# Kernel optimization log

Hardware: AMD Instinct MI355X
Metric: run time of the kernel (lower is better)

Reference implementation:

```python
import jax, jax.numpy as jnp
import numpy as np

L = 7          # num_gc_layers
H = 64         # hidden_channels
N = 100000     # nodes
E = 1000000    # edges
G = 512        # graphs in batch
ATOM_DIMS = [119, 5, 12, 12, 10, 6, 6, 2, 2]   # OGB full_atom_feature_dims
BOND_DIMS = [5, 6, 2]                          # OGB full_bond_feature_dims
EPS_GEN = 1e-7   # GENConv message eps
EPS_BN = 1e-5    # BatchNorm eps
ATOM_OFF = np.concatenate([[0], np.cumsum(ATOM_DIMS)[:-1]]).astype(np.int64)
BOND_OFF = np.concatenate([[0], np.cumsum(BOND_DIMS)[:-1]]).astype(np.int64)


def setup_inputs() -> dict:
    key = jax.random.key(0)
    ks = jax.random.split(key, 12)
    x = jax.random.randint(ks[0], (N, len(ATOM_DIMS)), 0, 2)
    edge_index = jax.random.randint(ks[1], (2, E), 0, N)
    edge_attr = jax.random.randint(ks[2], (E, len(BOND_DIMS)), 0, 2)
    batch = jnp.sort(jax.random.randint(ks[3], (N,), 0, G))
    s = 0.02
    w = 1.0 / np.sqrt(H).astype(np.float32)
    return {
        "atom_table": jax.random.normal(ks[4], (sum(ATOM_DIMS), H), jnp.float32) * s,
        "bond_table": jax.random.normal(ks[5], (sum(BOND_DIMS), H), jnp.float32) * s,
        "vn0": jnp.zeros((H,), jnp.float32),  # virtualnode embedding, const-init 0
        "gcn_W": jax.random.normal(ks[6], (L, H, H), jnp.float32) * w,
        "gcn_b": jnp.zeros((L, H), jnp.float32),
        "norm_gamma": jnp.ones((L, H), jnp.float32),
        "norm_beta": jnp.zeros((L, H), jnp.float32),
        "vn_W1": jax.random.normal(ks[7], (L - 1, H, H), jnp.float32) * w,
        "vn_b1": jnp.zeros((L - 1, H), jnp.float32),
        "vn_g1": jnp.ones((L - 1, H), jnp.float32),
        "vn_be1": jnp.zeros((L - 1, H), jnp.float32),
        "vn_W2": jax.random.normal(ks[8], (L - 1, H, H), jnp.float32) * w,
        "vn_b2": jnp.zeros((L - 1, H), jnp.float32),
        "vn_g2": jnp.ones((L - 1, H), jnp.float32),
        "vn_be2": jnp.zeros((L - 1, H), jnp.float32),
        "x": x,
        "edge_index": edge_index,
        "edge_attr": edge_attr,
        "batch": batch,
        "classification": 0,
    }


def _bn(h, g, b):
    # BatchNorm1d, training mode (biased batch stats over the node axis)
    mu = h.mean(0)
    var = h.var(0)
    return (h - mu) * jax.lax.rsqrt(var + EPS_BN) * g + b


def _genconv(h, src, dst, edge_emb, W, b):
    # GENConv, aggr='add', mlp_layers=1 (single last_lin Linear)
    msg = jax.nn.relu(h[src] + edge_emb) + EPS_GEN        # [E, H]
    m = jax.ops.segment_sum(msg, dst, num_segments=N)     # [N, H]
    return (h + m) @ W + b


def reference(atom_table, bond_table, vn0, gcn_W, gcn_b, norm_gamma, norm_beta,
              vn_W1, vn_b1, vn_g1, vn_be1, vn_W2, vn_b2, vn_g2, vn_be2,
              x, edge_index, edge_attr, batch, classification):
    # AtomEncoder / BondEncoder: sum of per-feature embeddings via offset table
    h = atom_table[x + jnp.asarray(ATOM_OFF)].sum(1)                   # [N, H]
    edge_emb = bond_table[edge_attr + jnp.asarray(BOND_OFF)].sum(1)    # [E, H]
    vn = jnp.broadcast_to(vn0[None, :], (G, H))                        # [G, H]
    h = h + vn[batch]
    src, dst = edge_index[0], edge_index[1]

    # block == 'res+': conv0, then [BN -> ReLU -> (vnode) -> conv -> +res]
    h = _genconv(h, src, dst, edge_emb, gcn_W[0], gcn_b[0])
    for l in range(1, L):
        h2 = jax.nn.relu(_bn(h, norm_gamma[l - 1], norm_beta[l - 1]))
        # virtual-node update: global_add_pool + 2-layer MLP (Lin-BN-ReLU x2)
        vt = jax.ops.segment_sum(h2, batch, num_segments=G) + vn
        z = jax.nn.relu(_bn(vt @ vn_W1[l - 1] + vn_b1[l - 1], vn_g1[l - 1], vn_be1[l - 1]))
        vn = jax.nn.relu(_bn(z @ vn_W2[l - 1] + vn_b2[l - 1], vn_g2[l - 1], vn_be2[l - 1]))
        h2 = h2 + vn[batch]
        h = _genconv(h2, src, dst, edge_emb, gcn_W[l], gcn_b[l]) + h
    h = _bn(h, norm_gamma[L - 1], norm_beta[L - 1])

    # classification=False -> global_mean_pool readout
    cnt = jax.ops.segment_sum(jnp.ones((N,), h.dtype), batch, num_segments=G)
    out = jax.ops.segment_sum(h, batch, num_segments=G) / jnp.clip(cnt, 1.0)[:, None]
    return out
```

## Files before the change

### kernel.cpp

```cpp
#include <hip/hip_runtime.h>
#include <hip/hip_bf16.h>
#include <hip/hip_fp16.h>

#define NN 100000
#define EE 1000000
#define GG 512
#define HH 64
#define LL 7
#define NH (NN*HH)
#define GH (GG*HH)
#define EPS_GEN 1e-7f
#define EPS_BN 1e-5f
#define SCAN_BLKS 98
#define SLOTS 64
#define CONV_BLOCKS 6250

typedef _Float16 half8  __attribute__((ext_vector_type(8)));
typedef _Float16 half4  __attribute__((ext_vector_type(4)));
typedef _Float16 half2v __attribute__((ext_vector_type(2)));
typedef float    float4v __attribute__((ext_vector_type(4)));

__device__ __constant__ int c_atom_off[9] = {0,119,124,136,148,158,164,170,172};

__global__ void k_atom_enc(const float* __restrict__ atom_table,
                           const float* __restrict__ vn0,
                           const int* __restrict__ x,
                           _Float16* __restrict__ h16) {
    int tid = blockIdx.x * blockDim.x + threadIdx.x;
    int n = tid >> 6, c = tid & 63;
    if (n >= NN) return;
    float acc = vn0[c];
    const int* xr = x + n * 9;
    #pragma unroll
    for (int f = 0; f < 9; ++f) acc += atom_table[(xr[f] + c_atom_off[f]) * HH + c];
    h16[tid] = (_Float16)acc;
}

__global__ void k_prep(const float* __restrict__ W, const float* __restrict__ bond,
                       _Float16* __restrict__ W16f, _Float16* __restrict__ ctab16) {
    int i = blockIdx.x * blockDim.x + threadIdx.x;
    if (i < LL * 4096) {
        int l = i / 4096, r = i % 4096;
        int j = r & 7, lane = (r >> 3) & 63, kh = (r >> 9) & 1, t = r >> 10;
        int q = (lane >> 4) & 3, c = lane & 15;
        W16f[i] = (_Float16)W[l * 4096 + (kh * 32 + q * 8 + j) * 64 + t * 16 + c];
    } else {
        int k = i - LL * 4096;
        if (k < 60 * 64) {
            int cmb = k >> 6, lane = k & 63;
            int a0 = cmb % 5, a1 = (cmb / 5) % 6, a2 = cmb / 30;
            ctab16[k] = (_Float16)(bond[a0 * 64 + lane] + bond[(5 + a1) * 64 + lane]
                                   + bond[(11 + a2) * 64 + lane]);
        }
    }
}

__global__ void k_count2(const int* __restrict__ edge_index, const int* __restrict__ edge_attr,
                         int* __restrict__ cur, unsigned int* __restrict__ recs) {
    int e = blockIdx.x * blockDim.x + threadIdx.x;
    if (e >= EE) return;
    int src = edge_index[e];
    int dst = edge_index[EE + e];
    int combo = edge_attr[e * 3] + 5 * edge_attr[e * 3 + 1] + 30 * edge_attr[e * 3 + 2];
    unsigned int rank = (unsigned int)atomicAdd(&cur[dst], 1);
    recs[e] = (unsigned int)src | ((unsigned int)combo << 17) | (rank << 23);
}

__global__ void k_scan1(const int* __restrict__ cnt, int* __restrict__ rp, int* __restrict__ part) {
    __shared__ int s[256];
    int t = threadIdx.x, blk = blockIdx.x;
    int base = blk * 1024 + t * 4;
    int v0 = 0, v1 = 0, v2 = 0, v3 = 0;
    if (base + 3 < NN) {
        int4 q = *(const int4*)(cnt + base);
        v0 = q.x; v1 = q.y; v2 = q.z; v3 = q.w;
    } else {
        if (base + 0 < NN) v0 = cnt[base + 0];
        if (base + 1 < NN) v1 = cnt[base + 1];
        if (base + 2 < NN) v2 = cnt[base + 2];
        if (base + 3 < NN) v3 = cnt[base + 3];
    }
    int s4 = v0 + v1 + v2 + v3;
    s[t] = s4;
    __syncthreads();
    for (int off = 1; off < 256; off <<= 1) {
        int x = (t >= off) ? s[t - off] : 0;
        __syncthreads();
        s[t] += x;
        __syncthreads();
    }
    int excl = s[t] - s4;
    if (t == 255) part[blk] = s[255];
    if (base + 0 < NN) rp[base + 0] = excl;
    if (base + 1 < NN) rp[base + 1] = excl + v0;
    if (base + 2 < NN) rp[base + 2] = excl + v0 + v1;
    if (base + 3 < NN) rp[base + 3] = excl + v0 + v1 + v2;
}

__global__ void k_scan2(int* __restrict__ part) {
    __shared__ int s[128];
    int t = threadIdx.x;
    int v = (t < SCAN_BLKS) ? part[t] : 0;
    s[t] = v;
    __syncthreads();
    for (int off = 1; off < 128; off <<= 1) {
        int x = (t >= off) ? s[t - off] : 0;
        __syncthreads();
        s[t] += x;
        __syncthreads();
    }
    if (t < SCAN_BLKS) part[t] = s[t] - v;
}

__global__ void k_scan3(int* __restrict__ rp, const int* __restrict__ part) {
    int i = blockIdx.x * blockDim.x + threadIdx.x;
    if (i < NN) rp[i] += part[i >> 10];
    if (i == 0) rp[NN] = EE;
}

__global__ void k_fill2(const int* __restrict__ edge_index, const unsigned int* __restrict__ recs,
                        const int* __restrict__ rp, unsigned int* __restrict__ edges) {
    int e = blockIdx.x * blockDim.x + threadIdx.x;
    if (e >= EE) return;
    unsigned int rec = recs[e];
    int dst = edge_index[EE + e];
    edges[rp[dst] + (rec >> 23)] = rec & 0x7FFFFFu;
}

__global__ __launch_bounds__(128, 8) void k_conv_mfma(
        const _Float16* __restrict__ h16, const float* res,
        const int* __restrict__ rp, const unsigned int* __restrict__ edges,
        const _Float16* __restrict__ ctab16, const _Float16* __restrict__ W16f,
        const float* __restrict__ bvec,
        float* __restrict__ out, float* __restrict__ statsPart) {
    __shared__ __align__(16) _Float16 sA[16 * 64];
    int lane = threadIdx.x & 63;
    int wv = threadIdx.x >> 6;
    int g  = lane >> 5;
    int sg = (lane >> 4) & 1;
    int cc = (lane & 15) * 4;
    int q = lane >> 4;
    int c = lane & 15;
    int n0 = blockIdx.x * 16;
    const half4 z4 = {(_Float16)0, (_Float16)0, (_Float16)0, (_Float16)0};

    const half8* wf = (const half8*)W16f;
    half8 bf[2][2];
    #pragma unroll
    for (int t = 0; t < 2; ++t) {
        bf[t][0] = wf[((wv * 2 + t) * 2 + 0) * 64 + lane];
        bf[t][1] = wf[((wv * 2 + t) * 2 + 1) * 64 + lane];
    }

    #pragma unroll 1
    for (int i = 0; i < 4; ++i) {
        int r_loc = wv * 8 + g * 4 + i;
        int n = n0 + r_loc;
        float ax = 0.f, ay = 0.f, az = 0.f, aw = 0.f;
        int beg = rp[n], end = rp[n + 1];
        int deg = end - beg;
        int j = beg;
        for (; j + 8 <= end; j += 8) {
            unsigned int rec[4];
            rec[0] = edges[j + sg];
            rec[1] = edges[j + 2 + sg];
            rec[2] = edges[j + 4 + sg];
            rec[3] = edges[j + 6 + sg];
            half4 hh[4], tt[4];
            #pragma unroll
            for (int u = 0; u < 4; ++u) {
                hh[u] = *(const half4*)(h16 + (size_t)(rec[u] & 0x1FFFF) * 64 + cc);
                tt[u] = *(const half4*)(ctab16 + ((rec[u] >> 17) & 63) * 64 + cc);
            }
            #pragma unroll
            for (int u = 0; u < 4; ++u) {
                half4 m = __builtin_elementwise_max(hh[u] + tt[u], z4);
                ax += (float)m[0]; ay += (float)m[1];
                az += (float)m[2]; aw += (float)m[3];
            }
        }
        for (; j < end; j += 4) {
            int i0 = j + sg, i1 = j + 2 + sg;
            bool v0 = i0 < end, v1 = i1 < end;
            unsigned int r0 = edges[v0 ? i0 : beg];
            unsigned int r1 = edges[v1 ? i1 : beg];
            half4 h0 = *(const half4*)(h16 + (size_t)(r0 & 0x1FFFF) * 64 + cc);
            half4 t0 = *(const half4*)(ctab16 + ((r0 >> 17) & 63) * 64 + cc);
            half4 h1 = *(const half4*)(h16 + (size_t)(r1 & 0x1FFFF) * 64 + cc);
            half4 t1 = *(const half4*)(ctab16 + ((r1 >> 17) & 63) * 64 + cc);
            half4 m0 = __builtin_elementwise_max(h0 + t0, z4);
            half4 m1 = __builtin_elementwise_max(h1 + t1, z4);
            if (v0) {
                ax += (float)m0[0]; ay += (float)m0[1];
                az += (float)m0[2]; aw += (float)m0[3];
            }
            if (v1) {
                ax += (float)m1[0]; ay += (float)m1[1];
                az += (float)m1[2]; aw += (float)m1[3];
            }
        }
        ax += __shfl_xor(ax, 16, 64); ay += __shfl_xor(ay, 16, 64);
        az += __shfl_xor(az, 16, 64); aw += __shfl_xor(aw, 16, 64);
        half4 sv = *(const half4*)(h16 + (size_t)n * 64 + cc);
        float ed = (float)deg * EPS_GEN;
        ax += (float)sv[0] + ed; ay += (float)sv[1] + ed;
        az += (float)sv[2] + ed; aw += (float)sv[3] + ed;
        if (sg == 0) {
            half4 pk;
            pk[0] = (_Float16)ax; pk[1] = (_Float16)ay;
            pk[2] = (_Float16)az; pk[3] = (_Float16)aw;
            *(half4*)(&sA[r_loc * 64 + cc]) = pk;
        }
    }
    __syncthreads();

    half8 af0 = *(const half8*)(sA + c * 64 + q * 8);
    half8 af1 = *(const half8*)(sA + c * 64 + 32 + q * 8);
    float4v d[2];
    #pragma unroll
    for (int t = 0; t < 2; ++t) {
        d[t] = (float4v){0.f, 0.f, 0.f, 0.f};
        d[t] = __builtin_amdgcn_mfma_f32_16x16x32_f16(af0, bf[t][0], d[t], 0, 0, 0);
        d[t] = __builtin_amdgcn_mfma_f32_16x16x32_f16(af1, bf[t][1], d[t], 0, 0, 0);
    }

    float ps[2], pq[2];
    #pragma unroll
    for (int t = 0; t < 2; ++t) { ps[t] = 0.f; pq[t] = 0.f; }
    #pragma unroll
    for (int t = 0; t < 2; ++t) {
        int tg = wv * 2 + t;
        float bz = bvec[tg * 16 + c];
        #pragma unroll
        for (int r = 0; r < 4; ++r) {
            int row = n0 + q * 4 + r;
            float val = d[t][r] + bz;
            size_t off = (size_t)row * 64 + tg * 16 + c;
            if (res) val += res[off];
            out[off] = val;
            ps[t] += val;
            pq[t] = fmaf(val, val, pq[t]);
        }
    }
    #pragma unroll
    for (int t = 0; t < 2; ++t) {
        ps[t] += __shfl_xor(ps[t], 16, 64); ps[t] += __shfl_xor(ps[t], 32, 64);
        pq[t] += __shfl_xor(pq[t], 16, 64); pq[t] += __shfl_xor(pq[t], 32, 64);
    }
    float* sp = statsPart + ((blockIdx.x * 2 + wv) & (SLOTS - 1)) * 128;
    if (lane < 16) {
        #pragma unroll
        for (int t = 0; t < 2; ++t) {
            int tg = wv * 2 + t;
            atomicAdd(&sp[tg * 16 + lane], ps[t]);
            atomicAdd(&sp[64 + tg * 16 + lane], pq[t]);
        }
    }
}


__global__ void k_bn_relu_vt2(const float* __restrict__ h, const float* __restrict__ spart,
                              const float* __restrict__ gamma, const float* __restrict__ beta,
                              const int* __restrict__ batch,
                              _Float16* __restrict__ h16, float* __restrict__ vt) {
    __shared__ float sTmp[256];
    __shared__ float sMS[128];
    {
        int ch = threadIdx.x & 127, hf = threadIdx.x >> 7;
        float a = 0.f;
        #pragma unroll 8
        for (int i = hf; i < SLOTS; i += 2) a += spart[i * 128 + ch];
        sTmp[threadIdx.x] = a;
    }
    __syncthreads();
    if (threadIdx.x < 64) {
        int c = threadIdx.x;
        float s = sTmp[c] + sTmp[128 + c];
        float q = sTmp[64 + c] + sTmp[192 + c];
        float mu = s * (1.f / NN);
        float var = q * (1.f / NN) - mu * mu;
        sMS[c] = mu;
        sMS[64 + c] = rsqrtf(var + EPS_BN);
    }
    __syncthreads();
    int lane = threadIdx.x & 63;
    int w = blockIdx.x * 4 + (threadIdx.x >> 6);
    int n0 = w * 8;
    if (n0 >= NN) return;
    int n1 = min(n0 + 8, NN);
    float mu = sMS[lane];
    float inv = sMS[64 + lane] * gamma[lane];
    float bet = beta[lane];
    float acc = 0.f;
    int gcur = batch[n0];
    for (int n = n0; n < n1; ++n) {
        float v = fmaxf((h[(size_t)n * 64 + lane] - mu) * inv + bet, 0.f);
        h16[(size_t)n * 64 + lane] = (_Float16)v;
        int g = batch[n];
        if (g != gcur) {
            atomicAdd(&vt[(size_t)gcur * 64 + lane], acc);
            acc = 0.f; gcur = g;
        }
        acc += v;
    }
    atomicAdd(&vt[(size_t)gcur * 64 + lane], acc);
}

__global__ void k_vn_gemm(float* __restrict__ in, int clear_in,
                          const float* in_stats, const float* in_g, const float* in_be,
                          const float* addmat, const float* add_stats,
                          const float* add_g, const float* add_be,
                          const float* addvec,
                          const float* __restrict__ W, const float* __restrict__ bvec,
                          float* __restrict__ out, float* __restrict__ out_stats) {
    __shared__ float sW[4096];
    __shared__ float sRed[2][4][64];
    for (int i = threadIdx.x; i < 4096; i += 256) sW[i] = W[i];
    __syncthreads();
    int lane = threadIdx.x & 63, wv = threadIdx.x >> 6;
    int w = blockIdx.x * 4 + wv;
    float imu = 0.f, iinv = 0.f, ibe = 0.f;
    if (in_stats) {
        float mu = in_stats[lane] * (1.f / GG);
        float var = in_stats[64 + lane] * (1.f / GG) - mu * mu;
        imu = mu; iinv = rsqrtf(var + EPS_BN) * in_g[lane]; ibe = in_be[lane];
    }
    float amu = 0.f, ainv = 0.f, abe = 0.f;
    if (addmat && add_stats) {
        float mu = add_stats[lane] * (1.f / GG);
        float var = add_stats[64 + lane] * (1.f / GG) - mu * mu;
        amu = mu; ainv = rsqrtf(var + EPS_BN) * add_g[lane]; abe = add_be[lane];
    }
    float av_const = addvec ? addvec[lane] : 0.f;
    float psum = 0.f, psq = 0.f;
    for (int r = w * 4; r < w * 4 + 4; ++r) {
        float va = in[r * 64 + lane];
        if (clear_in) in[r * 64 + lane] = 0.f;
        if (in_stats) va = fmaxf((va - imu) * iinv + ibe, 0.f);
        if (addmat) va += fmaxf((addmat[r * 64 + lane] - amu) * ainv + abe, 0.f);
        va += av_const;
        float acc = bvec[lane];
        #pragma unroll
        for (int k = 0; k < 64; ++k)
            acc = fmaf(__shfl(va, k, 64), sW[k * 64 + lane], acc);
        out[r * 64 + lane] = acc;
        psum += acc; psq = fmaf(acc, acc, psq);
    }
    sRed[0][wv][lane] = psum;
    sRed[1][wv][lane] = psq;
    __syncthreads();
    if (threadIdx.x < 64) {
        float s = 0.f, q = 0.f;
        #pragma unroll
        for (int i = 0; i < 4; ++i) { s += sRed[0][i][threadIdx.x]; q += sRed[1][i][threadIdx.x]; }
        atomicAdd(&out_stats[threadIdx.x], s);
        atomicAdd(&out_stats[64 + threadIdx.x], q);
    }
}

__global__ void k_addvn16(_Float16* __restrict__ h16, const float* __restrict__ t2,
                          const float* __restrict__ stats,
                          const float* __restrict__ g2, const float* __restrict__ be2,
                          const int* __restrict__ batch) {
    int tid = blockIdx.x * blockDim.x + threadIdx.x;
    int n = tid >> 4, p = tid & 15;
    if (n >= NN) return;
    int c0 = p * 4;
    float mu[4], iv[4], be[4];
    #pragma unroll
    for (int k = 0; k < 4; ++k) {
        int ci = c0 + k;
        float m = stats[ci] * (1.f / GG);
        float v = stats[64 + ci] * (1.f / GG) - m * m;
        mu[k] = m;
        iv[k] = rsqrtf(v + EPS_BN) * g2[ci];
        be[k] = be2[ci];
    }
    int g = batch[n];
    float4 t = *(const float4*)(t2 + (size_t)g * 64 + c0);
    float tv[4] = {t.x, t.y, t.z, t.w};
    half4 hv = *(half4*)(h16 + (size_t)n * 64 + c0);
    half4 o;
    #pragma unroll
    for (int k = 0; k < 4; ++k) {
        float a = fmaxf((tv[k] - mu[k]) * iv[k] + be[k], 0.f);
        o[k] = (_Float16)((float)hv[k] + a);
    }
    *(half4*)(h16 + (size_t)n * 64 + c0) = o;
}

__global__ void k_pool2(const float* __restrict__ h, const float* __restrict__ spart,
                        const float* __restrict__ gamma, const float* __restrict__ beta,
                        const int* __restrict__ batch,
                        float* __restrict__ out, float* __restrict__ cnt) {
    __shared__ float sTmp[256];
    __shared__ float sMS[128];
    {
        int ch = threadIdx.x & 127, hf = threadIdx.x >> 7;
        float a = 0.f;
        #pragma unroll 8
        for (int i = hf; i < SLOTS; i += 2) a += spart[i * 128 + ch];
        sTmp[threadIdx.x] = a;
    }
    __syncthreads();
    if (threadIdx.x < 64) {
        int c = threadIdx.x;
        float s = sTmp[c] + sTmp[128 + c];
        float q = sTmp[64 + c] + sTmp[192 + c];
        float mu = s * (1.f / NN);
        float var = q * (1.f / NN) - mu * mu;
        sMS[c] = mu;
        sMS[64 + c] = rsqrtf(var + EPS_BN);
    }
    __syncthreads();
    int lane = threadIdx.x & 63;
    int w = blockIdx.x * 4 + (threadIdx.x >> 6);
    int n0 = w * 16;
    if (n0 >= NN) return;
    int n1 = min(n0 + 16, NN);
    float mu = sMS[lane];
    float inv = sMS[64 + lane] * gamma[lane];
    float bet = beta[lane];
    float acc = 0.f;
    int run = 0;
    int gcur = batch[n0];
    for (int n = n0; n < n1; ++n) {
        float v = (h[(size_t)n * 64 + lane] - mu) * inv + bet;
        int g = batch[n];
        if (g != gcur) {
            atomicAdd(&out[(size_t)gcur * 64 + lane], acc);
            if (lane == 0) atomicAdd(&cnt[gcur], (float)run);
            acc = 0.f; run = 0; gcur = g;
        }
        acc += v; run++;
    }
    atomicAdd(&out[(size_t)gcur * 64 + lane], acc);
    if (lane == 0) atomicAdd(&cnt[gcur], (float)run);
}

__global__ void k_div(float* __restrict__ out, const float* __restrict__ cnt) {
    int tid = blockIdx.x * blockDim.x + threadIdx.x;
    if (tid >= GH) return;
    out[tid] /= fmaxf(cnt[tid >> 6], 1.0f);
}

extern "C" void kernel_launch(void* const* d_in, const int* in_sizes, int n_in,
                              void* d_out, int out_size, void* d_ws, size_t ws_size,
                              hipStream_t stream) {
    const float* atom_table = (const float*)d_in[0];
    const float* bond_table = (const float*)d_in[1];
    const float* vn0   = (const float*)d_in[2];
    const float* gcn_W = (const float*)d_in[3];
    const float* gcn_b = (const float*)d_in[4];
    const float* ng    = (const float*)d_in[5];
    const float* nb    = (const float*)d_in[6];
    const float* vn_W1 = (const float*)d_in[7];
    const float* vn_b1 = (const float*)d_in[8];
    const float* vn_g1 = (const float*)d_in[9];
    const float* vn_be1= (const float*)d_in[10];
    const float* vn_W2 = (const float*)d_in[11];
    const float* vn_b2 = (const float*)d_in[12];
    const float* vn_g2 = (const float*)d_in[13];
    const float* vn_be2= (const float*)d_in[14];
    const int* x          = (const int*)d_in[15];
    const int* edge_index = (const int*)d_in[16];
    const int* edge_attr  = (const int*)d_in[17];
    const int* batch      = (const int*)d_in[18];

    float* ws = (float*)d_ws;
    float* hB   = ws;
    _Float16* h16 = (_Float16*)(ws + (size_t)NH);
    float* vt   = ws + (size_t)NH + NH / 2;
    float* t1   = vt + GH;
    float* t2   = t1 + GH;
    float* convStatsP = t2 + GH;
    float* msAll      = convStatsP + 7 * SLOTS * 128;
    float* vn1Stats   = msAll + 7 * 128;
    float* vn2Stats   = vn1Stats + 6 * 128;
    float* cnt    = vn2Stats + 6 * 128;
    _Float16* ctab16 = (_Float16*)(cnt + GG);
    _Float16* W16f   = ctab16 + 60 * 64;
    int*   rp     = (int*)(W16f + LL * 4096);
    int*   cur    = rp + (NN + 2);
    int*   part   = cur + NN;
    unsigned int* edges = (unsigned int*)(part + 128);
    unsigned int* recs = (unsigned int*)h16;

    const int blkN = NH / 256;
    const int blkG = (GH + 255) / 256;
    const int blkE = (EE + 255) / 256;
    const int blkRL = ((NN + 7) / 8 + 3) / 4;
    const int blkPL = ((NN + 15) / 16 + 3) / 4;
    const int blkAV = (NN * 16) / 256;
    const int blkPR = (LL * 4096 + 60 * 64 + 255) / 256;
    float* outp = (float*)d_out;

    hipMemsetAsync(cur, 0, (size_t)NN * 4, stream);
    k_count2<<<blkE, 256, 0, stream>>>(edge_index, edge_attr, cur, recs);
    k_scan1<<<SCAN_BLKS, 256, 0, stream>>>(cur, rp, part);
    k_scan2<<<1, 128, 0, stream>>>(part);
    k_scan3<<<(NN + 255) / 256, 256, 0, stream>>>(rp, part);
    k_fill2<<<blkE, 256, 0, stream>>>(edge_index, recs, rp, edges);

    k_atom_enc<<<blkN, 256, 0, stream>>>(atom_table, vn0, x, h16);
    k_prep<<<blkPR, 256, 0, stream>>>(gcn_W, bond_table, W16f, ctab16);
    hipMemsetAsync(convStatsP, 0, (7 * SLOTS * 128 + 7 * 128 + 12 * 128) * 4, stream);
    hipMemsetAsync(vt, 0, (size_t)GH * 4, stream);

    k_conv_mfma<<<CONV_BLOCKS, 128, 0, stream>>>(h16, nullptr, rp, edges, ctab16, W16f,
                                                 gcn_b, hB, convStatsP);

    for (int l = 1; l < LL; ++l) {
        k_bn_relu_vt2<<<blkRL, 256, 0, stream>>>(hB, convStatsP + (size_t)(l - 1) * SLOTS * 128,
                                                 ng + (size_t)(l - 1) * HH,
                                                 nb + (size_t)(l - 1) * HH, batch, h16, vt);
        if (l == 1)
            k_vn_gemm<<<32, 256, 0, stream>>>(vt, 1, nullptr, nullptr, nullptr,
                                              nullptr, nullptr, nullptr, nullptr, vn0,
                                              vn_W1, vn_b1, t1, vn1Stats);
        else
            k_vn_gemm<<<32, 256, 0, stream>>>(vt, 1, nullptr, nullptr, nullptr,
                                              t2, vn2Stats + (size_t)(l - 2) * 128,
                                              vn_g2 + (size_t)(l - 2) * HH,
                                              vn_be2 + (size_t)(l - 2) * HH, nullptr,
                                              vn_W1 + (size_t)(l - 1) * 4096,
                                              vn_b1 + (size_t)(l - 1) * HH, t1,
                                              vn1Stats + (size_t)(l - 1) * 128);
        k_vn_gemm<<<32, 256, 0, stream>>>(t1, 0, vn1Stats + (size_t)(l - 1) * 128,
                                          vn_g1 + (size_t)(l - 1) * HH,
                                          vn_be1 + (size_t)(l - 1) * HH,
                                          nullptr, nullptr, nullptr, nullptr, nullptr,
                                          vn_W2 + (size_t)(l - 1) * 4096,
                                          vn_b2 + (size_t)(l - 1) * HH, t2,
                                          vn2Stats + (size_t)(l - 1) * 128);
        k_addvn16<<<blkAV, 256, 0, stream>>>(h16, t2, vn2Stats + (size_t)(l - 1) * 128,
                                             vn_g2 + (size_t)(l - 1) * HH,
                                             vn_be2 + (size_t)(l - 1) * HH, batch);

        k_conv_mfma<<<CONV_BLOCKS, 128, 0, stream>>>(h16, hB, rp, edges, ctab16,
                                                     W16f + (size_t)l * 4096,
                                                     gcn_b + (size_t)l * HH, hB,
                                                     convStatsP + (size_t)l * SLOTS * 128);
    }

    hipMemsetAsync(outp, 0, (size_t)GH * 4, stream);
    hipMemsetAsync(cnt, 0, (size_t)GG * 4, stream);
    k_pool2<<<blkPL, 256, 0, stream>>>(hB, convStatsP + (size_t)6 * SLOTS * 128,
                                       ng + (size_t)6 * HH, nb + (size_t)6 * HH,
                                       batch, outp, cnt);
    k_div<<<blkG, 256, 0, stream>>>(outp, cnt);
}
```

Before: 839.5 us.

## Give each wave its own 16-node tile in conv kernel, removing block barrier

Each wave now gathers and aggregates its own 16-node tile and runs the full 64-column MFMA transform itself, so the block-wide __syncthreads is replaced by a per-wave waitcnt and the launch uses half as many blocks. This removes cross-wave synchronisation stalls when degree imbalance makes one wave wait on another. In exchange each wave holds all four B fragments (more registers) and issues twice the MFMAs and stat atomics. Relying on s_waitcnt alone for intra-wave LDS visibility is assumed safe.

New measurement: 899.9 us. 7.2% more time.

```diff
diff --git a/kernel.cpp b/kernel.cpp
--- a/kernel.cpp
+++ b/kernel.cpp
@@ -13,7 +13,7 @@
 #define EPS_BN 1e-5f
 #define SCAN_BLKS 98
 #define SLOTS 64
-#define CONV_BLOCKS 6250
+#define CONV_BLOCKS 3125
 
 typedef _Float16 half8  __attribute__((ext_vector_type(8)));
 typedef _Float16 half4  __attribute__((ext_vector_type(4)));
@@ -133,28 +133,30 @@
         const _Float16* __restrict__ ctab16, const _Float16* __restrict__ W16f,
         const float* __restrict__ bvec,
         float* __restrict__ out, float* __restrict__ statsPart) {
-    __shared__ __align__(16) _Float16 sA[16 * 64];
+    __shared__ __align__(16) _Float16 sA[2][16 * 64];
     int lane = threadIdx.x & 63;
     int wv = threadIdx.x >> 6;
+    _Float16* sAw = sA[wv];
     int g  = lane >> 5;
     int sg = (lane >> 4) & 1;
     int cc = (lane & 15) * 4;
     int q = lane >> 4;
     int c = lane & 15;
-    int n0 = blockIdx.x * 16;
+    int tile = blockIdx.x * 2 + wv;
+    int n0 = tile * 16;
     const half4 z4 = {(_Float16)0, (_Float16)0, (_Float16)0, (_Float16)0};
 
     const half8* wf = (const half8*)W16f;
-    half8 bf[2][2];
-    #pragma unroll
-    for (int t = 0; t < 2; ++t) {
-        bf[t][0] = wf[((wv * 2 + t) * 2 + 0) * 64 + lane];
-        bf[t][1] = wf[((wv * 2 + t) * 2 + 1) * 64 + lane];
+    half8 bf[4][2];
+    #pragma unroll
+    for (int t = 0; t < 4; ++t) {
+        bf[t][0] = wf[(t * 2 + 0) * 64 + lane];
+        bf[t][1] = wf[(t * 2 + 1) * 64 + lane];
     }
 
     #pragma unroll 1
-    for (int i = 0; i < 4; ++i) {
-        int r_loc = wv * 8 + g * 4 + i;
+    for (int i = 0; i < 8; ++i) {
+        int r_loc = g * 8 + i;
         int n = n0 + r_loc;
         float ax = 0.f, ay = 0.f, az = 0.f, aw = 0.f;
         int beg = rp[n], end = rp[n + 1];
@@ -209,33 +211,32 @@
             half4 pk;
             pk[0] = (_Float16)ax; pk[1] = (_Float16)ay;
             pk[2] = (_Float16)az; pk[3] = (_Float16)aw;
-            *(half4*)(&sA[r_loc * 64 + cc]) = pk;
-        }
-    }
-    __syncthreads();
-
-    half8 af0 = *(const half8*)(sA + c * 64 + q * 8);
-    half8 af1 = *(const half8*)(sA + c * 64 + 32 + q * 8);
-    float4v d[2];
-    #pragma unroll
-    for (int t = 0; t < 2; ++t) {
+            *(half4*)(&sAw[r_loc * 64 + cc]) = pk;
+        }
+    }
+    __builtin_amdgcn_s_waitcnt(0);
+
+    half8 af0 = *(const half8*)(sAw + c * 64 + q * 8);
+    half8 af1 = *(const half8*)(sAw + c * 64 + 32 + q * 8);
+    float4v d[4];
+    #pragma unroll
+    for (int t = 0; t < 4; ++t) {
         d[t] = (float4v){0.f, 0.f, 0.f, 0.f};
         d[t] = __builtin_amdgcn_mfma_f32_16x16x32_f16(af0, bf[t][0], d[t], 0, 0, 0);
         d[t] = __builtin_amdgcn_mfma_f32_16x16x32_f16(af1, bf[t][1], d[t], 0, 0, 0);
     }
 
-    float ps[2], pq[2];
-    #pragma unroll
-    for (int t = 0; t < 2; ++t) { ps[t] = 0.f; pq[t] = 0.f; }
-    #pragma unroll
-    for (int t = 0; t < 2; ++t) {
-        int tg = wv * 2 + t;
-        float bz = bvec[tg * 16 + c];
+    float ps[4], pq[4];
+    #pragma unroll
+    for (int t = 0; t < 4; ++t) { ps[t] = 0.f; pq[t] = 0.f; }
+    #pragma unroll
+    for (int t = 0; t < 4; ++t) {
+        float bz = bvec[t * 16 + c];
         #pragma unroll
         for (int r = 0; r < 4; ++r) {
             int row = n0 + q * 4 + r;
             float val = d[t][r] + bz;
-            size_t off = (size_t)row * 64 + tg * 16 + c;
+            size_t off = (size_t)row * 64 + t * 16 + c;
             if (res) val += res[off];
             out[off] = val;
             ps[t] += val;
@@ -243,17 +244,16 @@
         }
     }
     #pragma unroll
-    for (int t = 0; t < 2; ++t) {
+    for (int t = 0; t < 4; ++t) {
         ps[t] += __shfl_xor(ps[t], 16, 64); ps[t] += __shfl_xor(ps[t], 32, 64);
         pq[t] += __shfl_xor(pq[t], 16, 64); pq[t] += __shfl_xor(pq[t], 32, 64);
     }
-    float* sp = statsPart + ((blockIdx.x * 2 + wv) & (SLOTS - 1)) * 128;
+    float* sp = statsPart + (tile & (SLOTS - 1)) * 128;
     if (lane < 16) {
         #pragma unroll
-        for (int t = 0; t < 2; ++t) {
-            int tg = wv * 2 + t;
-            atomicAdd(&sp[tg * 16 + lane], ps[t]);
-            atomicAdd(&sp[64 + tg * 16 + lane], pq[t]);
+        for (int t = 0; t < 4; ++t) {
+            atomicAdd(&sp[t * 16 + lane], ps[t]);
+            atomicAdd(&sp[64 + t * 16 + lane], pq[t]);
         }
     }
 }
```

## Stage combined bond table in LDS and broadcast edge records via shuffles

Applied to the files above, without the earlier changes.

The conv kernel now copies the 60-row combined edge-embedding table into shared memory once per block and reads edge embeddings from LDS instead of global memory. Edge records for up to 32 neighbors are loaded with one coalesced load per half-wave and distributed with __shfl, replacing the repeated per-edge global loads. The self-feature load is hoisted ahead of the gather loop. This adds 7.5KB of LDS per block plus an extra barrier, which may reduce occupancy, and adds shuffle overhead in the inner loop.

After: 781.2 us. 6.9% less time.

```diff
diff --git a/kernel.cpp b/kernel.cpp
--- a/kernel.cpp
+++ b/kernel.cpp
@@ -134,6 +134,7 @@
         const float* __restrict__ bvec,
         float* __restrict__ out, float* __restrict__ statsPart) {
     __shared__ __align__(16) _Float16 sA[16 * 64];
+    __shared__ __align__(16) _Float16 sC[60 * 64];
     int lane = threadIdx.x & 63;
     int wv = threadIdx.x >> 6;
     int g  = lane >> 5;
@@ -141,8 +142,12 @@
     int cc = (lane & 15) * 4;
     int q = lane >> 4;
     int c = lane & 15;
+    int lane32 = lane & 31;
     int n0 = blockIdx.x * 16;
     const half4 z4 = {(_Float16)0, (_Float16)0, (_Float16)0, (_Float16)0};
+
+    for (int i = threadIdx.x; i < 480; i += 128)
+        ((int4*)sC)[i] = ((const int4*)ctab16)[i];
 
     const half8* wf = (const half8*)W16f;
     half8 bf[2][2];
@@ -151,57 +156,56 @@
         bf[t][0] = wf[((wv * 2 + t) * 2 + 0) * 64 + lane];
         bf[t][1] = wf[((wv * 2 + t) * 2 + 1) * 64 + lane];
     }
+    __syncthreads();
 
     #pragma unroll 1
     for (int i = 0; i < 4; ++i) {
         int r_loc = wv * 8 + g * 4 + i;
         int n = n0 + r_loc;
-        float ax = 0.f, ay = 0.f, az = 0.f, aw = 0.f;
         int beg = rp[n], end = rp[n + 1];
         int deg = end - beg;
-        int j = beg;
-        for (; j + 8 <= end; j += 8) {
-            unsigned int rec[4];
-            rec[0] = edges[j + sg];
-            rec[1] = edges[j + 2 + sg];
-            rec[2] = edges[j + 4 + sg];
-            rec[3] = edges[j + 6 + sg];
-            half4 hh[4], tt[4];
-            #pragma unroll
-            for (int u = 0; u < 4; ++u) {
-                hh[u] = *(const half4*)(h16 + (size_t)(rec[u] & 0x1FFFF) * 64 + cc);
-                tt[u] = *(const half4*)(ctab16 + ((rec[u] >> 17) & 63) * 64 + cc);
+        half4 sv = *(const half4*)(h16 + (size_t)n * 64 + cc);
+        float ax = 0.f, ay = 0.f, az = 0.f, aw = 0.f;
+        #pragma unroll 1
+        for (int base = beg; base < end; base += 32) {
+            int idx = base + lane32;
+            idx = idx < end ? idx : end - 1;
+            unsigned int rl = edges[idx];
+            int m = end - base; if (m > 32) m = 32;
+            int t = 0;
+            for (; t + 8 <= m; t += 8) {
+                unsigned int r[4];
+                #pragma unroll
+                for (int u = 0; u < 4; ++u)
+                    r[u] = __shfl(rl, (g << 5) + t + 2 * u + sg, 64);
+                half4 hh[4], tt[4];
+                #pragma unroll
+                for (int u = 0; u < 4; ++u) {
+                    hh[u] = *(const half4*)(h16 + (size_t)(r[u] & 0x1FFFF) * 64 + cc);
+                    tt[u] = *(const half4*)(sC + ((r[u] >> 17) & 63) * 64 + cc);
+                }
+                #pragma unroll
+                for (int u = 0; u < 4; ++u) {
+                    half4 mm = __builtin_elementwise_max(hh[u] + tt[u], z4);
+                    ax += (float)mm[0]; ay += (float)mm[1];
+                    az += (float)mm[2]; aw += (float)mm[3];
+                }
             }
-            #pragma unroll
-            for (int u = 0; u < 4; ++u) {
-                half4 m = __builtin_elementwise_max(hh[u] + tt[u], z4);
-                ax += (float)m[0]; ay += (float)m[1];
-                az += (float)m[2]; aw += (float)m[3];
-            }
-        }
-        for (; j < end; j += 4) {
-            int i0 = j + sg, i1 = j + 2 + sg;
-            bool v0 = i0 < end, v1 = i1 < end;
-            unsigned int r0 = edges[v0 ? i0 : beg];
-            unsigned int r1 = edges[v1 ? i1 : beg];
-            half4 h0 = *(const half4*)(h16 + (size_t)(r0 & 0x1FFFF) * 64 + cc);
-            half4 t0 = *(const half4*)(ctab16 + ((r0 >> 17) & 63) * 64 + cc);
-            half4 h1 = *(const half4*)(h16 + (size_t)(r1 & 0x1FFFF) * 64 + cc);
-            half4 t1 = *(const half4*)(ctab16 + ((r1 >> 17) & 63) * 64 + cc);
-            half4 m0 = __builtin_elementwise_max(h0 + t0, z4);
-            half4 m1 = __builtin_elementwise_max(h1 + t1, z4);
-            if (v0) {
-                ax += (float)m0[0]; ay += (float)m0[1];
-                az += (float)m0[2]; aw += (float)m0[3];
-            }
-            if (v1) {
-                ax += (float)m1[0]; ay += (float)m1[1];
-                az += (float)m1[2]; aw += (float)m1[3];
+            for (; t < m; t += 2) {
+                int e0 = t + sg;
+                bool v0 = e0 < m;
+                unsigned int r0 = __shfl(rl, (g << 5) + (v0 ? e0 : 0), 64);
+                half4 h0 = *(const half4*)(h16 + (size_t)(r0 & 0x1FFFF) * 64 + cc);
+                half4 t0 = *(const half4*)(sC + ((r0 >> 17) & 63) * 64 + cc);
+                half4 m0 = __builtin_elementwise_max(h0 + t0, z4);
+                if (v0) {
+                    ax += (float)m0[0]; ay += (float)m0[1];
+                    az += (float)m0[2]; aw += (float)m0[3];
+                }
             }
         }
         ax += __shfl_xor(ax, 16, 64); ay += __shfl_xor(ay, 16, 64);
         az += __shfl_xor(az, 16, 64); aw += __shfl_xor(aw, 16, 64);
-        half4 sv = *(const half4*)(h16 + (size_t)n * 64 + cc);
         float ed = (float)deg * EPS_GEN;
         ax += (float)sv[0] + ed; ay += (float)sv[1] + ed;
         az += (float)sv[2] + ed; aw += (float)sv[3] + ed;
```
